# Kernel tuning notes

Hardware: AMD Instinct MI355X
Metric: run time of the kernel (lower is better)

## Reference

```python
import jax, jax.numpy as jnp
import numpy as np


def conv(x, w, b=None, stride=1, pad=0):
    out = jax.lax.conv_general_dilated(x, w, (stride, stride), [(pad, pad), (pad, pad)],
                                       dimension_numbers=('NCHW', 'OIHW', 'NCHW'))
    if b is not None:
        out = out + b[None, :, None, None]
    return out


def fsm(x, att_w, conv_w):
    # FeatureSelectionModule: global-avg-pool -> 1x1 conv -> sigmoid gate, residual, 1x1 proj
    gap = jnp.mean(x, axis=(2, 3), keepdims=True)
    atten = jax.nn.sigmoid(conv(gap, att_w))
    return conv(x + x * atten, conv_w)


def mdcn(x, offset, mask, weight, bias, pad=1, G=8):
    # Modulated deformable conv v2: stride 1, dilation 1, conv groups 1, G deformable groups.
    N, C, H, W = x.shape
    Co, Ci, kh, kw = weight.shape
    K = kh * kw
    Cg = C // G
    off = offset.reshape(N, G, 2, K, H, W)          # per-group (y, x) offsets per kernel tap
    msk = mask.reshape(N, G, 1, K, H, W)
    ky, kx = jnp.meshgrid(jnp.arange(kh), jnp.arange(kw), indexing='ij')
    py = (jnp.arange(H, dtype=x.dtype)[None, None, None, :, None] - pad) + ky.reshape(1, 1, K, 1, 1) + off[:, :, 0]
    px = (jnp.arange(W, dtype=x.dtype)[None, None, None, None, :] - pad) + kx.reshape(1, 1, K, 1, 1) + off[:, :, 1]
    y0 = jnp.floor(py)
    x0 = jnp.floor(px)
    wy1 = py - y0
    wy0 = 1.0 - wy1
    wx1 = px - x0
    wx0 = 1.0 - wx1
    xg = x.reshape(N, G, Cg, H * W)

    def gather(iy, ix):
        valid = (iy >= 0) & (iy <= H - 1) & (ix >= 0) & (ix <= W - 1)
        idx = (jnp.clip(iy, 0, H - 1) * W + jnp.clip(ix, 0, W - 1)).astype(jnp.int32)
        v = jnp.take_along_axis(xg, idx.reshape(N, G, 1, K * H * W), axis=3)
        return v.reshape(N, G, Cg, K, H, W) * valid[:, :, None].astype(x.dtype)

    val = ((wy0 * wx0)[:, :, None] * gather(y0, x0)
         + (wy0 * wx1)[:, :, None] * gather(y0, x0 + 1)
         + (wy1 * wx0)[:, :, None] * gather(y0 + 1, x0)
         + (wy1 * wx1)[:, :, None] * gather(y0 + 1, x0 + 1))
    val = val * msk                                   # [N,G,Cg,K,H,W]
    out = jnp.einsum('ngckhw,ogck->nohw', val, weight.reshape(Co, G, Cg, K))
    return out + bias[None, :, None, None]


def align(feat_l, feat_s, att_w, fsm_w, off_w, om_w, om_b, dcn_w, dcn_b):
    # FeatureAlign_V2
    N, Cs, H, W = feat_s.shape[0], feat_s.shape[1], feat_l.shape[2], feat_l.shape[3]
    feat_up = jax.image.resize(feat_s, (N, Cs, H, W), 'bilinear')  # align_corners=False
    feat_arm = fsm(feat_l, att_w, fsm_w)
    off_feat = conv(jnp.concatenate([feat_arm, feat_up * 2.0], axis=1), off_w)
    om = conv(off_feat, om_w, om_b, pad=1)            # conv_offset_mask: 3*G*K channels
    o1, o2, mk = jnp.split(om, 3, axis=1)
    offset = jnp.concatenate([o1, o2], axis=1)
    mask = jax.nn.sigmoid(mk)
    feat_align = jax.nn.relu(mdcn(feat_up, offset, mask, dcn_w, dcn_b))
    return feat_align + feat_arm


def setup_inputs() -> dict:
    key = jax.random.key(0)
    ks = iter(jax.random.split(key, 64))

    def w(shape):
        fan_in = shape[1] * shape[2] * shape[3]
        return jax.random.normal(next(ks), shape, jnp.float32) / np.float32(np.sqrt(fan_in))

    def b(n):
        return jnp.zeros((n,), jnp.float32)

    d = {}
    d['c2'] = jax.random.normal(next(ks), (1, 256, 128, 128), jnp.float32)
    d['c3'] = jax.random.normal(next(ks), (1, 512, 64, 64), jnp.float32)
    d['c4'] = jax.random.normal(next(ks), (1, 1024, 32, 32), jnp.float32)
    d['c5'] = jax.random.normal(next(ks), (1, 2048, 16, 16), jnp.float32)
    OC = 256
    OM = 8 * 3 * 9  # deformable_groups * (2 offsets + 1 mask) * k*k = 216
    for tag, in_nc in (('16', 1024), ('8', 512), ('4', 256)):
        d['att_w' + tag] = w((in_nc, in_nc, 1, 1))
        d['fsm_w' + tag] = w((OC, in_nc, 1, 1))
        d['off_w' + tag] = w((OC, 2 * OC, 1, 1))
        d['om_w' + tag] = w((OM, OC, 3, 3))
        d['om_b' + tag] = b(OM)
        d['dcn_w' + tag] = w((OC, OC, 3, 3))
        d['dcn_b' + tag] = b(OC)
        d['out_w' + tag] = w((OC, OC, 3, 3))
        d['out_b' + tag] = b(OC)
    d['lat_w'] = w((OC, 2048, 1, 1))
    d['lat_b'] = b(OC)
    return d


def reference(c2, c3, c4, c5,
              att_w16, fsm_w16, off_w16, om_w16, om_b16, dcn_w16, dcn_b16, out_w16, out_b16,
              att_w8, fsm_w8, off_w8, om_w8, om_b8, dcn_w8, dcn_b8, out_w8, out_b8,
              att_w4, fsm_w4, off_w4, om_w4, om_b4, dcn_w4, dcn_b4, out_w4, out_b4,
              lat_w, lat_b):
    # top-down pass, coarsest first (matches FAN.forward with reversed inputs)
    p5 = conv(c5, lat_w, lat_b)
    f16 = align(c4, p5, att_w16, fsm_w16, off_w16, om_w16, om_b16, dcn_w16, dcn_b16)
    p4 = conv(f16, out_w16, out_b16, pad=1)
    f8 = align(c3, f16, att_w8, fsm_w8, off_w8, om_w8, om_b8, dcn_w8, dcn_b8)
    p3 = conv(f8, out_w8, out_b8, pad=1)
    f4 = align(c2, f8, att_w4, fsm_w4, off_w4, om_w4, om_b4, dcn_w4, dcn_b4)
    p2 = conv(f4, out_w4, out_b4, pad=1)
    return (p2, p3, p4, p5)
```

## Files before the change

kernel.cpp:

```cpp
#include <hip/hip_runtime.h>
#include <hip/hip_bf16.h>

typedef __hip_bfloat16 bf16;
typedef __attribute__((ext_vector_type(8))) short bf16x8;
typedef __attribute__((ext_vector_type(4))) float floatx4;

__device__ __forceinline__ float b2f(bf16 v) { return __bfloat162float(v); }
__device__ __forceinline__ bf16 f2b(float v) { return __float2bfloat16(v); }
__device__ __forceinline__ float us2f(unsigned short u) {
  union { unsigned int i; float f; } v; v.i = ((unsigned int)u) << 16; return v.f;
}
__device__ __forceinline__ unsigned short f2us(float f) {
  bf16 h = f2b(f); return *(unsigned short*)&h;
}
__device__ __forceinline__ int xcd_swz(int hw, int nwg) {
  return (nwg & 7) ? hw : ((hw & 7) * (nwg >> 3) + (hw >> 3));
}

__global__ __launch_bounds__(256) void gap_kernel(const float* __restrict__ x,
                                                  float* __restrict__ gap,
                                                  int HW, float inv) {
  int c = blockIdx.x;
  const float* p = x + (size_t)c * HW;
  float s = 0.f;
  for (int i = threadIdx.x; i < HW; i += 256) s += p[i];
  __shared__ float red[256];
  red[threadIdx.x] = s;
  __syncthreads();
  for (int w = 128; w > 0; w >>= 1) {
    if (threadIdx.x < w) red[threadIdx.x] += red[threadIdx.x + w];
    __syncthreads();
  }
  if (threadIdx.x == 0) gap[c] = red[0] * inv;
}

__global__ __launch_bounds__(256) void atten_kernel(const float* __restrict__ w,
                                                    const float* __restrict__ gap,
                                                    float* __restrict__ scale, int Ci) {
  int wave = threadIdx.x >> 6, lane = threadIdx.x & 63;
  int o = blockIdx.x * 4 + wave;
  const float4* wr = (const float4*)(w + (size_t)o * Ci);
  const float4* g4 = (const float4*)gap;
  int n4 = Ci >> 2;
  float s = 0.f;
  for (int i = lane; i < n4; i += 64) {
    float4 a = wr[i], b = g4[i];
    s += a.x * b.x + a.y * b.y + a.z * b.z + a.w * b.w;
  }
#pragma unroll
  for (int off = 32; off > 0; off >>= 1) s += __shfl_down(s, off);
  if (lane == 0) scale[o] = 1.f + 1.f / (1.f + expf(-s));
}

__global__ __launch_bounds__(256) void upsample2x_nhwc_kernel(
    const bf16* __restrict__ src, bf16* __restrict__ dst, int Hs, int Ws) {
  int p = blockIdx.x;
  int c = threadIdx.x;
  int W = Ws * 2;
  int y = p / W, x = p - y * W;
  float fy = y * 0.5f - 0.25f;
  float fx = x * 0.5f - 0.25f;
  int y0 = (int)floorf(fy), x0 = (int)floorf(fx);
  float wy1 = fy - (float)y0, wx1 = fx - (float)x0;
  int y0c = min(max(y0, 0), Hs - 1);
  int y1c = min(max(y0 + 1, 0), Hs - 1);
  int x0c = min(max(x0, 0), Ws - 1);
  int x1c = min(max(x0 + 1, 0), Ws - 1);
  float v00 = b2f(src[(size_t)(y0c * Ws + x0c) * 256 + c]);
  float v01 = b2f(src[(size_t)(y0c * Ws + x1c) * 256 + c]);
  float v10 = b2f(src[(size_t)(y1c * Ws + x0c) * 256 + c]);
  float v11 = b2f(src[(size_t)(y1c * Ws + x1c) * 256 + c]);
  float v = (1.f - wy1) * ((1.f - wx1) * v00 + wx1 * v01)
          + wy1 * ((1.f - wx1) * v10 + wx1 * v11);
  dst[(size_t)p * 256 + c] = f2b(v);
}

__global__ __launch_bounds__(256) void packw1_kernel(const float* __restrict__ w,
                                                     bf16* __restrict__ BP, int K) {
  int idx = blockIdx.x * 256 + threadIdx.x;
  int j = idx & 7;
  int o = (idx >> 3) & 255;
  int kc8 = idx >> 11;
  int k = kc8 * 8 + j;
  BP[idx] = f2b(w[(size_t)o * K + k]);
}

__global__ __launch_bounds__(256) void pack_level_kernel(
    const float* __restrict__ fsm_w, int Ci,
    const float* __restrict__ off_w, const float* __restrict__ om_w,
    const float* __restrict__ dcn_w, const float* __restrict__ out_w,
    bf16* __restrict__ BPfsm, bf16* __restrict__ BPoff, bf16* __restrict__ BPom,
    bf16* __restrict__ BPdcn, bf16* __restrict__ BPout) {
  int b = blockIdx.x;
  if (b < Ci) {
    int idx = b * 256 + threadIdx.x;
    int j = idx & 7, o = (idx >> 3) & 255, k = (idx >> 11) * 8 + j;
    BPfsm[idx] = f2b(fsm_w[(size_t)o * Ci + k]);
    return;
  }
  b -= Ci;
  if (b < 512) {
    int idx = b * 256 + threadIdx.x;
    int j = idx & 7, o = (idx >> 3) & 255, k = (idx >> 11) * 8 + j;
    BPoff[idx] = f2b(off_w[(size_t)o * 512 + k]);
    return;
  }
  b -= 512;
  const float* w;
  bf16* BP;
  int Co;
  if (b < 2304) { w = om_w; BP = BPom; Co = 216; }
  else if (b < 4608) {
    int idx = (b - 2304) * 256 + threadIdx.x;
    int j = idx & 7, o = (idx >> 3) & 255;
    int k = (idx >> 11) * 8 + j;
    int tap = k >> 8, ci = k & 255;
    BPdcn[idx] = f2b(dcn_w[((size_t)o * 256 + ci) * 9 + tap]);
    return;
  } else { w = out_w; BP = BPout; Co = 256; b -= 2304; }
  int idx = (b % 2304) * 256 + threadIdx.x;
  int j = idx & 7;
  int t1 = idx >> 3;
  int o = t1 & 255;
  int t2 = t1 >> 8;
  int q = t2 & 3;
  int t3 = t2 >> 2;
  int tap = t3 % 9;
  int c = t3 / 9;
  int ci = c * 32 + q * 8 + j;
  float v = (o < Co) ? w[((size_t)o * 256 + ci) * 9 + tap] : 0.f;
  BP[idx] = f2b(v);
}

template <bool NCHW1, typename TA1>
__global__ __launch_bounds__(256) void conv1x1_mfma_kernel(
    const TA1* __restrict__ A1, const float* __restrict__ scaleA,
    const bf16* __restrict__ A2, float scaleB,
    int Ci1, int Ci2, int HW,
    const bf16* __restrict__ BP, const float* __restrict__ bias,
    float* __restrict__ out1, bf16* __restrict__ out2, int ns2) {
  __shared__ __align__(16) bf16 sA[1024];
  int p0 = blockIdx.x * 32;
  int tid = threadIdx.x;
  int pix = tid & 31, sub = tid >> 5;
  int pix2 = tid >> 3, sub8 = tid & 7;
  int lane = tid & 63, wave = tid >> 6;
  int pg = wave & 1, cg = wave >> 1;
  int q = lane >> 4, n = lane & 15;

  floatx4 acc[4];
#pragma unroll
  for (int nt = 0; nt < 4; ++nt) acc[nt] = (floatx4)0.f;

  int nch = (Ci1 + Ci2) >> 5;
  for (int kc = 0; kc < nch; ++kc) {
    int ci0 = kc << 5;
    if (NCHW1 && ci0 < Ci1) {
#pragma unroll
      for (int it = 0; it < 4; ++it) {
        int cil = it * 8 + sub;
        float x = (float)A1[(size_t)(ci0 + cil) * HW + p0 + pix];
        if (scaleA) x *= scaleA[ci0 + cil];
        sA[((cil >> 3) * 32 + pix) * 8 + (cil & 7)] = f2b(x);
      }
    } else {
      const bf16* src; int cb; bool scl;
      if (!NCHW1 && ci0 < Ci1) {
        src = (const bf16*)(const void*)A1; cb = ci0; scl = false;
      } else {
        src = A2; cb = ci0 - Ci1; scl = true;
      }
      ushort4 raw = *(const ushort4*)&src[(size_t)(p0 + pix2) * 256 + cb + sub8 * 4];
      if (scl) {
        raw.x = f2us(us2f(raw.x) * scaleB);
        raw.y = f2us(us2f(raw.y) * scaleB);
        raw.z = f2us(us2f(raw.z) * scaleB);
        raw.w = f2us(us2f(raw.w) * scaleB);
      }
      *(ushort4*)&sA[((sub8 >> 1) * 32 + pix2) * 8 + (sub8 & 1) * 4] = raw;
    }
    __syncthreads();
    bf16x8 a = *(const bf16x8*)&sA[(q * 32 + pg * 16 + n) * 8];
    const bf16* bp = BP + ((size_t)(kc * 4 + q) * 256 + blockIdx.y * 128 + cg * 64) * 8;
#pragma unroll
    for (int nt = 0; nt < 4; ++nt) {
      bf16x8 b = *(const bf16x8*)&bp[(nt * 16 + n) * 8];
      acc[nt] = __builtin_amdgcn_mfma_f32_16x16x32_bf16(a, b, acc[nt], 0, 0, 0);
    }
    __syncthreads();
  }

  int pbase = p0 + pg * 16 + q * 4;
#pragma unroll
  for (int nt = 0; nt < 4; ++nt) {
    int o = blockIdx.y * 128 + cg * 64 + nt * 16 + n;
    float bv = bias ? bias[o] : 0.f;
#pragma unroll
    for (int r = 0; r < 4; ++r) {
      float v = acc[nt][r] + bv;
      if (out1) out1[(size_t)o * HW + pbase + r] = v;
      if (out2) out2[(size_t)(pbase + r) * ns2 + o] = f2b(v);
    }
  }
}

template <bool NCHW1, typename TA1>
__global__ __launch_bounds__(256) void conv1x1_split_kernel(
    const TA1* __restrict__ A1, const float* __restrict__ scaleA,
    const bf16* __restrict__ A2, float scaleB,
    int Ci1, int HW,
    const bf16* __restrict__ BP, float* __restrict__ PART, int kcPerZ) {
  __shared__ __align__(16) bf16 sA[1024];
  int p0 = blockIdx.x * 32;
  int tid = threadIdx.x;
  int pix = tid & 31, sub = tid >> 5;
  int pix2 = tid >> 3, sub8 = tid & 7;
  int lane = tid & 63, wave = tid >> 6;
  int pg = wave & 1, cg = wave >> 1;
  int q = lane >> 4, n = lane & 15;

  floatx4 acc[4];
#pragma unroll
  for (int nt = 0; nt < 4; ++nt) acc[nt] = (floatx4)0.f;

  int kc0 = blockIdx.z * kcPerZ;
  for (int kcl = 0; kcl < kcPerZ; ++kcl) {
    int kc = kc0 + kcl;
    int ci0 = kc << 5;
    if (NCHW1 && ci0 < Ci1) {
#pragma unroll
      for (int it = 0; it < 4; ++it) {
        int cil = it * 8 + sub;
        float x = (float)A1[(size_t)(ci0 + cil) * HW + p0 + pix];
        if (scaleA) x *= scaleA[ci0 + cil];
        sA[((cil >> 3) * 32 + pix) * 8 + (cil & 7)] = f2b(x);
      }
    } else {
      const bf16* src; int cb; bool scl;
      if (!NCHW1 && ci0 < Ci1) {
        src = (const bf16*)(const void*)A1; cb = ci0; scl = false;
      } else {
        src = A2; cb = ci0 - Ci1; scl = true;
      }
      ushort4 raw = *(const ushort4*)&src[(size_t)(p0 + pix2) * 256 + cb + sub8 * 4];
      if (scl) {
        raw.x = f2us(us2f(raw.x) * scaleB);
        raw.y = f2us(us2f(raw.y) * scaleB);
        raw.z = f2us(us2f(raw.z) * scaleB);
        raw.w = f2us(us2f(raw.w) * scaleB);
      }
      *(ushort4*)&sA[((sub8 >> 1) * 32 + pix2) * 8 + (sub8 & 1) * 4] = raw;
    }
    __syncthreads();
    bf16x8 a = *(const bf16x8*)&sA[(q * 32 + pg * 16 + n) * 8];
    const bf16* bp = BP + ((size_t)(kc * 4 + q) * 256 + blockIdx.y * 128 + cg * 64) * 8;
#pragma unroll
    for (int nt = 0; nt < 4; ++nt) {
      bf16x8 b = *(const bf16x8*)&bp[(nt * 16 + n) * 8];
      acc[nt] = __builtin_amdgcn_mfma_f32_16x16x32_bf16(a, b, acc[nt], 0, 0, 0);
    }
    __syncthreads();
  }

  int pbase = p0 + pg * 16 + q * 4;
#pragma unroll
  for (int nt = 0; nt < 4; ++nt) {
    int o = blockIdx.y * 128 + cg * 64 + nt * 16 + n;
#pragma unroll
    for (int r = 0; r < 4; ++r)
      PART[((size_t)blockIdx.z * 256 + o) * HW + pbase + r] = acc[nt][r];
  }
}

__global__ __launch_bounds__(256) void reduce_p5_kernel(
    const float* __restrict__ PART, const float* __restrict__ bias,
    float* __restrict__ out1, bf16* __restrict__ out2, int HW, int KS) {
  int o = blockIdx.x;
  int p = threadIdx.x;
  float s = bias[o];
  for (int z = 0; z < KS; ++z) s += PART[((size_t)z * 256 + o) * HW + p];
  out1[(size_t)o * HW + p] = s;
  out2[(size_t)p * 256 + o] = f2b(s);
}

__global__ __launch_bounds__(256) void reduce_nhwc_kernel(
    const float* __restrict__ PART, bf16* __restrict__ out2,
    int HW, int KS, int ns2) {
  int o = blockIdx.x;
  for (int p = threadIdx.x; p < HW; p += 256) {
    float s = 0.f;
    for (int z = 0; z < KS; ++z) s += PART[((size_t)z * 256 + o) * HW + p];
    out2[(size_t)p * ns2 + o] = f2b(s);
  }
}

template <int S>
__global__ __launch_bounds__(256) void conv3x3v2_kernel(
    const bf16* __restrict__ in, const bf16* __restrict__ BP,
    const float* __restrict__ bias,
    int H, int W, int Co,
    float* __restrict__ out1, bf16* __restrict__ out2, int ns2) {
  constexpr int P = 32 * S + 2;
  constexpr int TASKS = 3 * P * 8;
  constexpr int ITS = (TASKS + 255) / 256;
  __shared__ __align__(16) bf16 sA[2][4 * 3 * P * 8];
  int HW = H * W;
  int segs = W / (32 * S);
  int y = blockIdx.x / segs;
  int x0 = (blockIdx.x - y * segs) * (32 * S);
  int tid = threadIdx.x;
  int lane = tid & 63, wave = tid >> 6;
  int pg = wave & 1, cg = wave >> 1;
  int q = lane >> 4, n = lane & 15;
  int ob = blockIdx.y * 64 + cg * 32;

  int dstIdx[ITS], srcOff[ITS];
  bool act[ITS], val[ITS];
#pragma unroll
  for (int it = 0; it < ITS; ++it) {
    int tt = it * 256 + tid;
    act[it] = (tt < TASKS);
    int sub8 = tt & 7;
    int rp = tt >> 3;
    int row = rp / P;
    int pxl = rp - row * P;
    int yy = y + row - 1;
    int xg = x0 + pxl - 1;
    bool v = act[it] && ((unsigned)yy < (unsigned)H) && ((unsigned)xg < (unsigned)W);
    val[it] = v;
    srcOff[it] = v ? ((yy * W + xg) * 256 + sub8 * 4) : 0;
    dstIdx[it] = (((sub8 >> 1) * 3 + row) * P + pxl) * 8 + (sub8 & 1) * 4;
  }

  ushort4 pv[ITS];
  auto load_regs = [&](int kc) {
    int cb = kc << 5;
#pragma unroll
    for (int it = 0; it < ITS; ++it) {
      ushort4 z = {0, 0, 0, 0};
      pv[it] = val[it] ? *(const ushort4*)&in[(size_t)srcOff[it] + cb] : z;
    }
  };
  auto store_lds = [&](int buf) {
#pragma unroll
    for (int it = 0; it < ITS; ++it)
      if (act[it]) *(ushort4*)&sA[buf][dstIdx[it]] = pv[it];
  };

  floatx4 acc[S][2];
#pragma unroll
  for (int s = 0; s < S; ++s)
#pragma unroll
    for (int nt = 0; nt < 2; ++nt) acc[s][nt] = (floatx4)0.f;

  load_regs(0);
  store_lds(0);
  __syncthreads();
  load_regs(1);

  for (int kc = 0; kc < 8; ++kc) {
    const bf16* sv = &sA[kc & 1][0];
    const bf16* bpc = BP + (size_t)kc * 73728;
#pragma unroll
    for (int tap = 0; tap < 9; ++tap) {
      int ty = tap / 3, tx = tap % 3;
      bf16x8 a[S];
#pragma unroll
      for (int s = 0; s < S; ++s)
        a[s] = *(const bf16x8*)&sv[((q * 3 + ty) * P + tx + s * 32 + pg * 16 + n) * 8];
      const bf16* bp = bpc + ((size_t)(tap * 4 + q) * 256 + ob) * 8;
#pragma unroll
      for (int nt = 0; nt < 2; ++nt) {
        bf16x8 b = *(const bf16x8*)&bp[(nt * 16 + n) * 8];
#pragma unroll
        for (int s = 0; s < S; ++s)
          acc[s][nt] = __builtin_amdgcn_mfma_f32_16x16x32_bf16(a[s], b, acc[s][nt], 0, 0, 0);
      }
    }
    if (kc < 7) {
      store_lds((kc + 1) & 1);
      __syncthreads();
      if (kc < 6) load_regs(kc + 2);
    }
  }

#pragma unroll
  for (int s = 0; s < S; ++s) {
    int pbase = y * W + x0 + s * 32 + pg * 16 + q * 4;
#pragma unroll
    for (int nt = 0; nt < 2; ++nt) {
      int o = ob + nt * 16 + n;
      if (o < Co) {
        float bv = bias ? bias[o] : 0.f;
#pragma unroll
        for (int r = 0; r < 4; ++r) {
          float v = acc[s][nt][r] + bv;
          if (out1) out1[(size_t)o * HW + pbase + r] = v;
          if (out2) out2[(size_t)(pbase + r) * ns2 + o] = f2b(v);
        }
      }
    }
  }
}

__global__ __launch_bounds__(512, 4) void mdcn_mfma_kernel(
    const bf16* __restrict__ UPn, const bf16* __restrict__ OM,
    const bf16* __restrict__ BP, const float* __restrict__ dcn_b,
    const bf16* __restrict__ ARM, bf16* __restrict__ F,
    int H, int W, int wshift) {
  __shared__ __align__(16) bf16 sval[2][32 * 272];
  __shared__ float4 mw[2304];
  __shared__ int mi[2304];
  int pb = xcd_swz(blockIdx.x, gridDim.x) * 32;
  int tid = threadIdx.x;

  for (int t2 = tid; t2 < 2304; t2 += 512) {
    int px_ = t2 & 31, g = (t2 >> 5) & 7, tap = t2 >> 8;
    int ky = tap / 3, kx = tap - ky * 3;
    int p = pb + px_;
    int y = p >> wshift, x = p & (W - 1);
    const bf16* omp = OM + (size_t)p * 216;
    float dy = b2f(omp[g * 18 + tap]);
    float dx = b2f(omp[g * 18 + 9 + tap]);
    float mm = 1.f / (1.f + expf(-b2f(omp[144 + g * 9 + tap])));
    float fpy = (float)(y - 1 + ky) + dy;
    float fpx = (float)(x - 1 + kx) + dx;
    fpy = fminf(fmaxf(fpy, -1.0e4f), 1.0e4f);
    fpx = fminf(fmaxf(fpx, -1.0e4f), 1.0e4f);
    float fy0 = floorf(fpy), fx0 = floorf(fpx);
    float wy1 = fpy - fy0, wx1 = fpx - fx0;
    float wy0 = 1.f - wy1, wx0 = 1.f - wx1;
    int iy0 = (int)fy0, ix0 = (int)fx0;
    bool vy0 = (unsigned)iy0 < (unsigned)H;
    bool vy1 = (unsigned)(iy0 + 1) < (unsigned)H;
    bool vx0 = (unsigned)ix0 < (unsigned)W;
    bool vx1 = (unsigned)(ix0 + 1) < (unsigned)W;
    float w00 = (vy0 && vx0) ? mm * wy0 * wx0 : 0.f;
    float w01 = (vy0 && vx1) ? mm * wy0 * wx1 : 0.f;
    float w10 = (vy1 && vx0) ? mm * wy1 * wx0 : 0.f;
    float w11 = (vy1 && vx1) ? mm * wy1 * wx1 : 0.f;
    int iy0c = min(max(iy0, 0), H - 1);
    int iy1c = min(max(iy0 + 1, 0), H - 1);
    int ix0c = min(max(ix0, 0), W - 1);
    int ix1c = min(max(ix0 + 1, 0), W - 1);
    mw[t2] = make_float4(w00, w01, w10, w11);
    mi[t2] = (iy0c * W + ix0c) | ((ix1c - ix0c) << 20) | ((iy1c - iy0c) << 21);
  }
  __syncthreads();

  int l4 = tid & 7;
  int px = (tid >> 3) & 31;
  int gh = tid >> 8;
  int lane = tid & 63, wave = tid >> 6;
  int q = lane >> 4, n = lane & 15;
  int rowb = l4 >> 1;
  int woff = px * 8 + (l4 & 1) * 4;

  floatx4 acc[2][2];
#pragma unroll
  for (int m = 0; m < 2; ++m)
#pragma unroll
    for (int nt = 0; nt < 2; ++nt) acc[m][nt] = (floatx4)0.f;

  ushort4 gl[4][4];
  auto gatherLoad = [&](int t) {
    int base = t * 256 + px + gh * 128;
#pragma unroll
    for (int gg = 0; gg < 4; ++gg) {
      int g = gh * 4 + gg;
      int mv = mi[base + gg * 32];
      int idx = mv & 0x3FFFF;
      int dxs = (mv >> 20) & 1;
      int dyW = ((mv >> 21) & 1) * W;
      const bf16* up = UPn + (size_t)idx * 256 + g * 32 + l4 * 4;
      gl[gg][0] = *(const ushort4*)(up);
      gl[gg][1] = *(const ushort4*)(up + dxs * 256);
      gl[gg][2] = *(const ushort4*)(up + dyW * 256);
      gl[gg][3] = *(const ushort4*)(up + (dyW + dxs) * 256);
    }
  };
  auto gatherStore = [&](int t) {
    bf16* sv = &sval[t & 1][0];
    int base = t * 256 + px + gh * 128;
#pragma unroll
    for (int gg = 0; gg < 4; ++gg) {
      int g = gh * 4 + gg;
      float4 wv = mw[base + gg * 32];
      ushort4 u00 = gl[gg][0], u01 = gl[gg][1], u10 = gl[gg][2], u11 = gl[gg][3];
      ushort4 o4;
      o4.x = f2us(wv.x * us2f(u00.x) + wv.y * us2f(u01.x)
                + wv.z * us2f(u10.x) + wv.w * us2f(u11.x));
      o4.y = f2us(wv.x * us2f(u00.y) + wv.y * us2f(u01.y)
                + wv.z * us2f(u10.y) + wv.w * us2f(u11.y));
      o4.z = f2us(wv.x * us2f(u00.z) + wv.y * us2f(u01.z)
                + wv.z * us2f(u10.z) + wv.w * us2f(u11.z));
      o4.w = f2us(wv.x * us2f(u00.w) + wv.y * us2f(u01.w)
                + wv.z * us2f(u10.w) + wv.w * us2f(u11.w));
      *(ushort4*)&sv[(g * 4 + rowb) * 272 + woff] = o4;
    }
  };

  gatherLoad(0);
  gatherStore(0);
  for (int t = 0; t < 9; ++t) {
    __syncthreads();
    if (t < 8) gatherLoad(t + 1);
    const bf16* sv = &sval[t & 1][0];
    const bf16* bpt = BP + ((size_t)(t * 32) * 256 + wave * 32) * 8;
#pragma unroll
    for (int kc = 0; kc < 8; ++kc) {
      int R = kc * 4 + q;
      bf16x8 a0 = *(const bf16x8*)&sv[R * 272 + n * 8];
      bf16x8 a1 = *(const bf16x8*)&sv[R * 272 + (16 + n) * 8];
      const bf16* bp = bpt + (size_t)R * 2048;
      bf16x8 b0 = *(const bf16x8*)&bp[n * 8];
      bf16x8 b1 = *(const bf16x8*)&bp[(16 + n) * 8];
      acc[0][0] = __builtin_amdgcn_mfma_f32_16x16x32_bf16(a0, b0, acc[0][0], 0, 0, 0);
      acc[0][1] = __builtin_amdgcn_mfma_f32_16x16x32_bf16(a0, b1, acc[0][1], 0, 0, 0);
      acc[1][0] = __builtin_amdgcn_mfma_f32_16x16x32_bf16(a1, b0, acc[1][0], 0, 0, 0);
      acc[1][1] = __builtin_amdgcn_mfma_f32_16x16x32_bf16(a1, b1, acc[1][1], 0, 0, 0);
    }
    if (t < 8) gatherStore(t + 1);
  }

#pragma unroll
  for (int m = 0; m < 2; ++m) {
#pragma unroll
    for (int nt = 0; nt < 2; ++nt) {
      int o = wave * 32 + nt * 16 + n;
      float bv = dcn_b[o];
#pragma unroll
      for (int r = 0; r < 4; ++r) {
        int p = pb + m * 16 + q * 4 + r;
        float v = fmaxf(acc[m][nt][r] + bv, 0.f) + b2f(ARM[(size_t)p * 256 + o]);
        F[(size_t)p * 256 + o] = f2b(v);
      }
    }
  }
}

__global__ __launch_bounds__(512, 1) void mdcn64_mfma_kernel(
    const bf16* __restrict__ UPn, const bf16* __restrict__ OM,
    const bf16* __restrict__ BP, const float* __restrict__ dcn_b,
    const bf16* __restrict__ ARM, bf16* __restrict__ F,
    int H, int W, int wshift) {
  __shared__ __align__(16) bf16 sval[2][32 * 520];
  __shared__ float4 mw2[2][512];
  __shared__ int mi2[2][512];
  int pb = xcd_swz(blockIdx.x, gridDim.x) * 64;
  int tid = threadIdx.x;
  int l4 = tid & 7;
  int px = tid >> 3;
  int gm = tid >> 6;
  int pxm = tid & 63;
  int lane = tid & 63, wave = tid >> 6;
  int q = lane >> 4, n = lane & 15;
  int rowb = l4 >> 1;
  int woff = px * 8 + (l4 & 1) * 4;

  int pM = pb + pxm;
  int yM = pM >> wshift, xM = pM & (W - 1);
  const bf16* ompM = OM + (size_t)pM * 216 + gm * 18;
  const bf16* ommM = OM + (size_t)pM * 216 + 144 + gm * 9;
  int slot = gm * 64 + pxm;

  auto metaCompute = [&](int t, int buf) {
    int ky = t / 3, kx = t - ky * 3;
    float dy = b2f(ompM[t]);
    float dx = b2f(ompM[9 + t]);
    float mm = 1.f / (1.f + expf(-b2f(ommM[t])));
    float fpy = (float)(yM - 1 + ky) + dy;
    float fpx = (float)(xM - 1 + kx) + dx;
    fpy = fminf(fmaxf(fpy, -1.0e4f), 1.0e4f);
    fpx = fminf(fmaxf(fpx, -1.0e4f), 1.0e4f);
    float fy0 = floorf(fpy), fx0 = floorf(fpx);
    float wy1 = fpy - fy0, wx1 = fpx - fx0;
    float wy0 = 1.f - wy1, wx0 = 1.f - wx1;
    int iy0 = (int)fy0, ix0 = (int)fx0;
    bool vy0 = (unsigned)iy0 < (unsigned)H;
    bool vy1 = (unsigned)(iy0 + 1) < (unsigned)H;
    bool vx0 = (unsigned)ix0 < (unsigned)W;
    bool vx1 = (unsigned)(ix0 + 1) < (unsigned)W;
    float w00 = (vy0 && vx0) ? mm * wy0 * wx0 : 0.f;
    float w01 = (vy0 && vx1) ? mm * wy0 * wx1 : 0.f;
    float w10 = (vy1 && vx0) ? mm * wy1 * wx0 : 0.f;
    float w11 = (vy1 && vx1) ? mm * wy1 * wx1 : 0.f;
    int iy0c = min(max(iy0, 0), H - 1);
    int iy1c = min(max(iy0 + 1, 0), H - 1);
    int ix0c = min(max(ix0, 0), W - 1);
    int ix1c = min(max(ix0 + 1, 0), W - 1);
    mw2[buf][slot] = make_float4(w00, w01, w10, w11);
    mi2[buf][slot] = (iy0c * W + ix0c) | ((ix1c - ix0c) << 20) | ((iy1c - iy0c) << 21);
  };

  floatx4 acc[4][2];
#pragma unroll
  for (int m = 0; m < 4; ++m)
#pragma unroll
    for (int nt = 0; nt < 2; ++nt) acc[m][nt] = (floatx4)0.f;

  ushort4 gl[8][4];
  auto gatherLoad = [&](int t) {
    int bufI = t & 1;
#pragma unroll
    for (int g = 0; g < 8; ++g) {
      int mv = mi2[bufI][g * 64 + px];
      int idx = mv & 0x3FFFF;
      int dxs = (mv >> 20) & 1;
      int dyW = ((mv >> 21) & 1) * W;
      const bf16* up = UPn + (size_t)idx * 256 + g * 32 + l4 * 4;
      gl[g][0] = *(const ushort4*)(up);
      gl[g][1] = *(const ushort4*)(up + dxs * 256);
      gl[g][2] = *(const ushort4*)(up + dyW * 256);
      gl[g][3] = *(const ushort4*)(up + (dyW + dxs) * 256);
    }
  };
  auto gatherStore = [&](int t) {
    bf16* sv = &sval[t & 1][0];
    int bufI = t & 1;
#pragma unroll
    for (int g = 0; g < 8; ++g) {
      float4 wv = mw2[bufI][g * 64 + px];
      ushort4 u00 = gl[g][0], u01 = gl[g][1], u10 = gl[g][2], u11 = gl[g][3];
      ushort4 o4;
      o4.x = f2us(wv.x * us2f(u00.x) + wv.y * us2f(u01.x)
                + wv.z * us2f(u10.x) + wv.w * us2f(u11.x));
      o4.y = f2us(wv.x * us2f(u00.y) + wv.y * us2f(u01.y)
                + wv.z * us2f(u10.y) + wv.w * us2f(u11.y));
      o4.z = f2us(wv.x * us2f(u00.z) + wv.y * us2f(u01.z)
                + wv.z * us2f(u10.z) + wv.w * us2f(u11.z));
      o4.w = f2us(wv.x * us2f(u00.w) + wv.y * us2f(u01.w)
                + wv.z * us2f(u10.w) + wv.w * us2f(u11.w));
      *(ushort4*)&sv[(g * 4 + rowb) * 520 + woff] = o4;
    }
  };

  metaCompute(0, 0);
  metaCompute(1, 1);
  __syncthreads();
  gatherLoad(0);
  gatherStore(0);

  for (int t = 0; t < 9; ++t) {
    __syncthreads();
    if (t < 8) gatherLoad(t + 1);
    if (t < 7) metaCompute(t + 2, t & 1);
    const bf16* sv = &sval[t & 1][0];
    const bf16* bpt = BP + ((size_t)(t * 32) * 256 + wave * 32) * 8;
#pragma unroll
    for (int kc = 0; kc < 8; ++kc) {
      int R = kc * 4 + q;
      const bf16* bp = bpt + (size_t)R * 2048;
      bf16x8 b0 = *(const bf16x8*)&bp[n * 8];
      bf16x8 b1 = *(const bf16x8*)&bp[(16 + n) * 8];
#pragma unroll
      for (int m = 0; m < 4; ++m) {
        bf16x8 a = *(const bf16x8*)&sv[R * 520 + (m * 16 + n) * 8];
        acc[m][0] = __builtin_amdgcn_mfma_f32_16x16x32_bf16(a, b0, acc[m][0], 0, 0, 0);
        acc[m][1] = __builtin_amdgcn_mfma_f32_16x16x32_bf16(a, b1, acc[m][1], 0, 0, 0);
      }
    }
    if (t < 8) gatherStore(t + 1);
  }

#pragma unroll
  for (int m = 0; m < 4; ++m) {
#pragma unroll
    for (int nt = 0; nt < 2; ++nt) {
      int o = wave * 32 + nt * 16 + n;
      float bv = dcn_b[o];
#pragma unroll
      for (int r = 0; r < 4; ++r) {
        int p = pb + m * 16 + q * 4 + r;
        float v = fmaxf(acc[m][nt][r] + bv, 0.f) + b2f(ARM[(size_t)p * 256 + o]);
        F[(size_t)p * 256 + o] = f2b(v);
      }
    }
  }
}

extern "C" void kernel_launch(void* const* d_in, const int* in_sizes, int n_in,
                              void* d_out, int out_size, void* d_ws, size_t ws_size,
                              hipStream_t stream) {
  const float* c2 = (const float*)d_in[0];
  const float* c3 = (const float*)d_in[1];
  const float* c4 = (const float*)d_in[2];
  const float* c5 = (const float*)d_in[3];
  const float* lat_w = (const float*)d_in[31];
  const float* lat_b = (const float*)d_in[32];
  float* out = (float*)d_out;
  (void)ws_size; (void)in_sizes; (void)n_in; (void)out_size;

  const size_t p2_off = 0;
  const size_t p3_off = 4194304;
  const size_t p4_off = p3_off + 1048576;
  const size_t p5_off = p4_off + 262144;

  char* ws = (char*)d_ws;
  bf16* UPn = (bf16*)(ws);
  bf16* ARM = (bf16*)(ws + 8388608);
  bf16* FB  = (bf16*)(ws + 16777216);
  bf16* P5N = (bf16*)(ws + 25165824);
  bf16* BPout = (bf16*)(ws + 25296896);
  bf16* BPfsm = (bf16*)(ws + 26476544);
  bf16* BPoff = (bf16*)(ws + 27000832);
  float* GAP = (float*)(ws + 27262976);
  float* SC  = (float*)(ws + 27271168);
  bf16* OM = (bf16*)(out + p2_off);
  bf16* BPom = (bf16*)((char*)(out + p2_off) + 10485760);
  bf16* BPdcn = (bf16*)((char*)(out + p2_off) + 11665408);
  float* PARTL = (float*)(out + p2_off);
  float* PART = (float*)ws;

  packw1_kernel<<<2048, 256, 0, stream>>>(lat_w, BPout, 2048);
  conv1x1_split_kernel<true, float><<<dim3(8, 2, 8), 256, 0, stream>>>(
      c5, nullptr, nullptr, 0.f, 2048, 256, BPout, PART, 8);
  reduce_p5_kernel<<<256, 256, 0, stream>>>(PART, lat_b, out + p5_off, P5N, 256, 8);

  struct Lv {
    const float* featl; int Ci; int H; int W; int wshift;
    float* pdst; int wbase;
  };
  Lv levels[3] = {
      {c4, 1024, 32, 32, 5, out + p4_off, 4},
      {c3, 512, 64, 64, 6, out + p3_off, 13},
      {c2, 256, 128, 128, 7, out + p2_off, 22},
  };

  for (int li = 0; li < 3; ++li) {
    const Lv& L = levels[li];
    const float* att_w = (const float*)d_in[L.wbase + 0];
    const float* fsm_w = (const float*)d_in[L.wbase + 1];
    const float* off_w = (const float*)d_in[L.wbase + 2];
    const float* om_w  = (const float*)d_in[L.wbase + 3];
    const float* om_b  = (const float*)d_in[L.wbase + 4];
    const float* dcn_w = (const float*)d_in[L.wbase + 5];
    const float* dcn_b = (const float*)d_in[L.wbase + 6];
    const float* out_w = (const float*)d_in[L.wbase + 7];
    const float* out_b = (const float*)d_in[L.wbase + 8];
    int HW = L.H * L.W;

    pack_level_kernel<<<L.Ci + 512 + 3 * 2304, 256, 0, stream>>>(
        fsm_w, L.Ci, off_w, om_w, dcn_w, out_w,
        BPfsm, BPoff, BPom, BPdcn, BPout);
    upsample2x_nhwc_kernel<<<HW, 256, 0, stream>>>(
        (li == 0) ? P5N : FB, UPn, L.H / 2, L.W / 2);
    gap_kernel<<<L.Ci, 256, 0, stream>>>(L.featl, GAP, HW, 1.f / (float)HW);
    atten_kernel<<<L.Ci / 4, 256, 0, stream>>>(att_w, GAP, SC, L.Ci);
    if (li == 0) {
      conv1x1_split_kernel<true, float><<<dim3(HW / 32, 2, 4), 256, 0, stream>>>(
          L.featl, SC, nullptr, 0.f, L.Ci, HW, BPfsm, PARTL, 8);
      reduce_nhwc_kernel<<<256, 256, 0, stream>>>(PARTL, ARM, HW, 4, 256);
    } else {
      conv1x1_mfma_kernel<true, float><<<dim3(HW / 32, 2), 256, 0, stream>>>(
          L.featl, SC, nullptr, 0.f, L.Ci, 0, HW, BPfsm, nullptr,
          nullptr, ARM, 256);
    }
    if (li == 0) {
      conv1x1_split_kernel<false, bf16><<<dim3(HW / 32, 2, 2), 256, 0, stream>>>(
          ARM, nullptr, UPn, 2.f, 256, HW, BPoff, PARTL, 8);
      reduce_nhwc_kernel<<<256, 256, 0, stream>>>(PARTL, FB, HW, 2, 256);
    } else {
      conv1x1_mfma_kernel<false, bf16><<<dim3(HW / 32, 2), 256, 0, stream>>>(
          ARM, nullptr, UPn, 2.f, 256, 256, HW, BPoff, nullptr,
          nullptr, FB, 256);
    }
    if (li == 2)
      conv3x3v2_kernel<2><<<dim3(HW / 64, 4), 256, 0, stream>>>(
          FB, BPom, om_b, L.H, L.W, 216, nullptr, OM, 216);
    else
      conv3x3v2_kernel<1><<<dim3(HW / 32, 4), 256, 0, stream>>>(
          FB, BPom, om_b, L.H, L.W, 216, nullptr, OM, 216);
    if (li == 2)
      mdcn64_mfma_kernel<<<HW / 64, 512, 0, stream>>>(
          UPn, OM, BPdcn, dcn_b, ARM, FB, L.H, L.W, L.wshift);
    else
      mdcn_mfma_kernel<<<HW / 32, 512, 0, stream>>>(
          UPn, OM, BPdcn, dcn_b, ARM, FB, L.H, L.W, L.wshift);
    if (li == 2)
      conv3x3v2_kernel<2><<<dim3(HW / 64, 4), 256, 0, stream>>>(
          FB, BPout, out_b, L.H, L.W, 256, L.pdst, nullptr, 256);
    else
      conv3x3v2_kernel<1><<<dim3(HW / 32, 4), 256, 0, stream>>>(
          FB, BPout, out_b, L.H, L.W, 256, L.pdst, nullptr, 256);
  }
}
```

Measured before the change: 639.7 us.

## Keep deformable sampling metadata in registers and share via wave shuffles

Each thread now computes the bilinear weights and packed indices for its own pixel/group pair and keeps them in registers, double-buffered as A/B copies. Other lanes in the wave read them with __shfl instead of going through shared-memory metadata arrays. Removing those arrays cuts LDS use and removes a block-wide barrier from the prologue. Launch bounds are raised to allow two 512-thread blocks per CU. The trade-offs are extra shuffle instructions and tighter register pressure, which risks spills with the large gl[8][4] staging buffer.

```diff
diff --git a/kernel.cpp b/kernel.cpp
--- a/kernel.cpp
+++ b/kernel.cpp
@@ -539,32 +539,28 @@
   }
 }
 
-__global__ __launch_bounds__(512, 1) void mdcn64_mfma_kernel(
+__global__ __launch_bounds__(512, 2) void mdcn64_mfma_kernel(
     const bf16* __restrict__ UPn, const bf16* __restrict__ OM,
     const bf16* __restrict__ BP, const float* __restrict__ dcn_b,
     const bf16* __restrict__ ARM, bf16* __restrict__ F,
     int H, int W, int wshift) {
   __shared__ __align__(16) bf16 sval[2][32 * 520];
-  __shared__ float4 mw2[2][512];
-  __shared__ int mi2[2][512];
   int pb = xcd_swz(blockIdx.x, gridDim.x) * 64;
   int tid = threadIdx.x;
   int l4 = tid & 7;
   int px = tid >> 3;
-  int gm = tid >> 6;
-  int pxm = tid & 63;
   int lane = tid & 63, wave = tid >> 6;
   int q = lane >> 4, n = lane & 15;
   int rowb = l4 >> 1;
   int woff = px * 8 + (l4 & 1) * 4;
-
-  int pM = pb + pxm;
+  int lbase = lane & 56;
+
+  int pM = pb + px;
   int yM = pM >> wshift, xM = pM & (W - 1);
-  const bf16* ompM = OM + (size_t)pM * 216 + gm * 18;
-  const bf16* ommM = OM + (size_t)pM * 216 + 144 + gm * 9;
-  int slot = gm * 64 + pxm;
-
-  auto metaCompute = [&](int t, int buf) {
+  const bf16* ompM = OM + (size_t)pM * 216 + l4 * 18;
+  const bf16* ommM = OM + (size_t)pM * 216 + 144 + l4 * 9;
+
+  auto metaCompute = [&](int t, float4& mwR, int& miR) {
     int ky = t / 3, kx = t - ky * 3;
     float dy = b2f(ompM[t]);
     float dx = b2f(ompM[9 + t]);
@@ -581,16 +577,15 @@
     bool vy1 = (unsigned)(iy0 + 1) < (unsigned)H;
     bool vx0 = (unsigned)ix0 < (unsigned)W;
     bool vx1 = (unsigned)(ix0 + 1) < (unsigned)W;
-    float w00 = (vy0 && vx0) ? mm * wy0 * wx0 : 0.f;
-    float w01 = (vy0 && vx1) ? mm * wy0 * wx1 : 0.f;
-    float w10 = (vy1 && vx0) ? mm * wy1 * wx0 : 0.f;
-    float w11 = (vy1 && vx1) ? mm * wy1 * wx1 : 0.f;
+    mwR.x = (vy0 && vx0) ? mm * wy0 * wx0 : 0.f;
+    mwR.y = (vy0 && vx1) ? mm * wy0 * wx1 : 0.f;
+    mwR.z = (vy1 && vx0) ? mm * wy1 * wx0 : 0.f;
+    mwR.w = (vy1 && vx1) ? mm * wy1 * wx1 : 0.f;
     int iy0c = min(max(iy0, 0), H - 1);
     int iy1c = min(max(iy0 + 1, 0), H - 1);
     int ix0c = min(max(ix0, 0), W - 1);
     int ix1c = min(max(ix0 + 1, 0), W - 1);
-    mw2[buf][slot] = make_float4(w00, w01, w10, w11);
-    mi2[buf][slot] = (iy0c * W + ix0c) | ((ix1c - ix0c) << 20) | ((iy1c - iy0c) << 21);
+    miR = (iy0c * W + ix0c) | ((ix1c - ix0c) << 20) | ((iy1c - iy0c) << 21);
   };
 
   floatx4 acc[4][2];
@@ -600,11 +595,10 @@
     for (int nt = 0; nt < 2; ++nt) acc[m][nt] = (floatx4)0.f;
 
   ushort4 gl[8][4];
-  auto gatherLoad = [&](int t) {
-    int bufI = t & 1;
+  auto gatherLoad = [&](int& miR) {
 #pragma unroll
     for (int g = 0; g < 8; ++g) {
-      int mv = mi2[bufI][g * 64 + px];
+      int mv = __shfl(miR, lbase | g);
       int idx = mv & 0x3FFFF;
       int dxs = (mv >> 20) & 1;
       int dyW = ((mv >> 21) & 1) * W;
@@ -615,12 +609,15 @@
       gl[g][3] = *(const ushort4*)(up + (dyW + dxs) * 256);
     }
   };
-  auto gatherStore = [&](int t) {
+  auto gatherStore = [&](int t, float4& mwR) {
     bf16* sv = &sval[t & 1][0];
-    int bufI = t & 1;
 #pragma unroll
     for (int g = 0; g < 8; ++g) {
-      float4 wv = mw2[bufI][g * 64 + px];
+      float4 wv;
+      wv.x = __shfl(mwR.x, lbase | g);
+      wv.y = __shfl(mwR.y, lbase | g);
+      wv.z = __shfl(mwR.z, lbase | g);
+      wv.w = __shfl(mwR.w, lbase | g);
       ushort4 u00 = gl[g][0], u01 = gl[g][1], u10 = gl[g][2], u11 = gl[g][3];
       ushort4 o4;
       o4.x = f2us(wv.x * us2f(u00.x) + wv.y * us2f(u01.x)
@@ -635,16 +632,22 @@
     }
   };
 
-  metaCompute(0, 0);
-  metaCompute(1, 1);
-  __syncthreads();
-  gatherLoad(0);
-  gatherStore(0);
+  float4 mwA, mwB;
+  int miA, miB;
+  metaCompute(0, mwA, miA);
+  gatherLoad(miA);
+  metaCompute(1, mwB, miB);
+  gatherStore(0, mwA);
 
   for (int t = 0; t < 9; ++t) {
     __syncthreads();
-    if (t < 8) gatherLoad(t + 1);
-    if (t < 7) metaCompute(t + 2, t & 1);
+    if (t < 8) {
+      if ((t + 1) & 1) gatherLoad(miB); else gatherLoad(miA);
+    }
+    if (t < 7) {
+      if ((t + 2) & 1) metaCompute(t + 2, mwB, miB);
+      else metaCompute(t + 2, mwA, miA);
+    }
     const bf16* sv = &sval[t & 1][0];
     const bf16* bpt = BP + ((size_t)(t * 32) * 256 + wave * 32) * 8;
 #pragma unroll
@@ -660,7 +663,9 @@
         acc[m][1] = __builtin_amdgcn_mfma_f32_16x16x32_bf16(a, b1, acc[m][1], 0, 0, 0);
       }
     }
-    if (t < 8) gatherStore(t + 1);
+    if (t < 8) {
+      if ((t + 1) & 1) gatherStore(t + 1, mwB); else gatherStore(t + 1, mwA);
+    }
   }
 
 #pragma unroll
```

Result: slower. 676.4 us (+5.7%).
